# Kernel optimization log

Hardware: AMD Instinct MI355X
Metric: run time of the kernel (lower is better)

Reference implementation:

```python
import jax, jax.numpy as jnp
import numpy as np

N = 50_000
E = 1_600_000
C_IN, C_HID, C_OUT, M = 128, 128, 2, 4


def gcn_norm(edge_index, num_nodes):
    # GCNConv default: add self-loops, symmetric normalization D^-1/2 (A+I) D^-1/2
    src, dst = edge_index[0], edge_index[1]
    loop = jnp.arange(num_nodes, dtype=edge_index.dtype)
    src = jnp.concatenate([src, loop])
    dst = jnp.concatenate([dst, loop])
    deg = jax.ops.segment_sum(jnp.ones_like(dst, dtype=jnp.float32), dst,
                              num_segments=num_nodes)
    dinv = jnp.where(deg > 0, jax.lax.rsqrt(deg), 0.0)
    norm = dinv[src] * dinv[dst]  # [E+N]
    return src, dst, norm


def propagate(h, src, dst, norm, num_nodes):
    # gather -> scale -> scatter-add (the memory-bound core)
    return jax.ops.segment_sum(h[src] * norm[:, None], dst, num_segments=num_nodes)


def setup_inputs() -> dict:
    key = jax.random.key(0)
    k0, k1, k2, k3 = jax.random.split(key, 4)
    x = jax.random.normal(k0, (N, C_IN), dtype=jnp.float32)
    edge_index = jax.random.randint(k1, (2, E), 0, N, dtype=jnp.int32)
    W1 = jax.random.normal(k2, (C_IN, C_HID), dtype=jnp.float32) * (1.0 / np.sqrt(C_IN))
    b1 = jnp.zeros((C_HID,), dtype=jnp.float32)
    W_out = jax.random.normal(k3, (M, C_HID, C_OUT), dtype=jnp.float32) * (1.0 / np.sqrt(C_HID))
    b_out = jnp.zeros((M, C_OUT), dtype=jnp.float32)
    return {"x": x, "edge_index": edge_index, "W1": W1, "b1": b1,
            "W_out": W_out, "b_out": b_out}


def reference(x, edge_index, W1, b1, W_out, b_out):
    n = x.shape[0]
    src, dst, norm = gcn_norm(edge_index, n)
    # hidden GCNConv + ReLU
    h = x @ W1                                  # [N, C_HID]
    h = propagate(h, src, dst, norm, n) + b1    # [N, C_HID]
    h = jax.nn.relu(h)
    # m output GCNConv heads. GCN propagation is linear in features, so
    # A_hat(h W_m) == (A_hat h) W_m: share one graph traversal across heads.
    agg = propagate(h, src, dst, norm, n)       # [N, C_HID]
    out = jnp.einsum('nf,mfo->mno', agg, W_out) + b_out[:, None, :]  # [M, N, C_OUT]
    return out
```

## Files before the change

### kernel.cpp

```cpp
#include <hip/hip_runtime.h>


constexpr int CIN = 128;
constexpr int BSHIFT = 6;
constexpr int NBLKB = 256;
constexpr int NBUK_MAX = 1024;
constexpr int CSR_CAP = 4096;

__device__ inline unsigned pack_bf16x2(float a, float b) {
  unsigned ua = __float_as_uint(a), ub = __float_as_uint(b);
  ua = (ua + 0x7FFFu + ((ua >> 16) & 1u)) >> 16;
  ub = (ub + 0x7FFFu + ((ub >> 16) & 1u)) >> 16;
  return ua | (ub << 16);
}
__device__ inline float bf_lo(unsigned u) { return __uint_as_float(u << 16); }
__device__ inline float bf_hi(unsigned u) { return __uint_as_float(u & 0xFFFF0000u); }

__global__ __launch_bounds__(256) void histbuck_k(const int* __restrict__ dst,
    int* __restrict__ blockhist, int E, int nbuk) {
  __shared__ int lh[NBUK_MAX];
  int b = blockIdx.x, t = threadIdx.x;
  for (int k = t; k < nbuk; k += 256) lh[k] = 0;
  __syncthreads();
  int per = (E + gridDim.x - 1) / gridDim.x;
  int s0 = b * per, s1 = min(E, s0 + per);
  for (int i = s0 + t; i < s1; i += 256) atomicAdd(&lh[dst[i] >> BSHIFT], 1);
  __syncthreads();
  for (int k = t; k < nbuk; k += 256) blockhist[k * NBLKB + b] = lh[k];
}

__global__ void scan_k(const int* __restrict__ v_in,
    int* __restrict__ excl_out, int* __restrict__ btot, int n) {
  __shared__ int wsum[16];
  int t = threadIdx.x, l = t & 63, w = t >> 6;
  int nw = blockDim.x >> 6;
  int i = blockIdx.x * blockDim.x + t;
  int v = (i < n) ? v_in[i] : 0;
  int orig = v;
  #pragma unroll
  for (int off = 1; off < 64; off <<= 1) {
    int u = __shfl_up(v, off);
    if (l >= off) v += u;
  }
  if (l == 63) wsum[w] = v;
  __syncthreads();
  int add = 0;
  for (int j = 0; j < nw; ++j) if (j < w) add += wsum[j];
  v += add;
  if (i < n) excl_out[i] = v - orig;
  if (t == (int)blockDim.x - 1 && btot != nullptr) btot[blockIdx.x] = v;
}

__global__ void scanfix2_k(int* __restrict__ soff, const int* __restrict__ boff, int n) {
  int i = blockIdx.x * 256 + threadIdx.x;
  if (i < n) soff[i] += boff[blockIdx.x];
}

__global__ __launch_bounds__(256) void stageB_k(const int* __restrict__ src,
    const int* __restrict__ dst, const int* __restrict__ soff,
    unsigned* __restrict__ stage, int E, int nbuk) {
  __shared__ int loff[NBUK_MAX];
  int b = blockIdx.x, t = threadIdx.x;
  for (int k = t; k < nbuk; k += 256) loff[k] = soff[k * NBLKB + b];
  __syncthreads();
  int per = (E + gridDim.x - 1) / gridDim.x;
  int s0 = b * per, s1 = min(E, s0 + per);
  for (int i = s0 + t; i < s1; i += 256) {
    int d = dst[i], s = src[i];
    int pos = atomicAdd(&loff[d >> BSHIFT], 1);
    stage[pos] = (unsigned)s | ((unsigned)(d & 63) << 17);
  }
}

__global__ __launch_bounds__(256) void csrloc_k(const unsigned* __restrict__ stage,
    const int* __restrict__ soff, int* __restrict__ row_ptr, int* __restrict__ csr,
    float* __restrict__ dinv, int N, int E, int nbuk) {
  __shared__ int cnt64[64], off64[64], cur64[64];
  __shared__ unsigned ebuf[CSR_CAP];
  __shared__ int sbuf[CSR_CAP];
  int k = blockIdx.x, t = threadIdx.x;
  if (t < 64) { cnt64[t] = 0; cur64[t] = 0; }
  __syncthreads();
  int r0 = soff[k * NBLKB];
  int r1 = (k + 1 < nbuk) ? soff[(k + 1) * NBLKB] : E;
  int len = r1 - r0;
  if (len <= CSR_CAP) {
    for (int i = t; i < len; i += 256) {
      unsigned s = stage[r0 + i];
      ebuf[i] = s;
      atomicAdd(&cnt64[s >> 17], 1);
    }
    __syncthreads();
    if (t < 64) {
      int v = cnt64[t], orig = v;
      #pragma unroll
      for (int off = 1; off < 64; off <<= 1) {
        int u = __shfl_up(v, off);
        if (t >= off) v += u;
      }
      off64[t] = v - orig;
      int n = (k << BSHIFT) + t;
      if (n < N) {
        row_ptr[n] = r0 + v - orig;
        dinv[n] = rsqrtf((float)(orig + 1));
      }
      if (k == nbuk - 1 && t == 63) row_ptr[N] = E;
    }
    __syncthreads();
    for (int i = t; i < len; i += 256) {
      unsigned s = ebuf[i];
      int dl = s >> 17;
      int pos = off64[dl] + atomicAdd(&cur64[dl], 1);
      sbuf[pos] = (int)(s & 0x1FFFF);
    }
    __syncthreads();
    for (int i = t; i < len; i += 256) csr[r0 + i] = sbuf[i];
  } else {
    for (int i = r0 + t; i < r1; i += 256) atomicAdd(&cnt64[stage[i] >> 17], 1);
    __syncthreads();
    if (t < 64) {
      int v = cnt64[t], orig = v;
      #pragma unroll
      for (int off = 1; off < 64; off <<= 1) {
        int u = __shfl_up(v, off);
        if (t >= off) v += u;
      }
      off64[t] = v - orig;
      int n = (k << BSHIFT) + t;
      if (n < N) {
        row_ptr[n] = r0 + v - orig;
        dinv[n] = rsqrtf((float)(orig + 1));
      }
      if (k == nbuk - 1 && t == 63) row_ptr[N] = E;
    }
    __syncthreads();
    for (int i = r0 + t; i < r1; i += 256) {
      unsigned s = stage[i];
      int dl = s >> 17;
      int pos = r0 + off64[dl] + atomicAdd(&cur64[dl], 1);
      csr[pos] = (int)(s & 0x1FFFF);
    }
  }
}

__global__ __launch_bounds__(256) void gemm_k(const float* __restrict__ x,
    const float* __restrict__ W, const float* __restrict__ dinv,
    unsigned* __restrict__ gu, int nrows) {
  __shared__ float As[32][132];
  __shared__ float Bs[32][132];
  int t = threadIdx.x;
  int tx = t & 15, ty = t >> 4;
  int row0 = blockIdx.x * 128;
  float acc[8][8];
  #pragma unroll
  for (int i = 0; i < 8; ++i)
    #pragma unroll
    for (int j = 0; j < 8; ++j) acc[i][j] = 0.f;

  for (int kc = 0; kc < 4; ++kc) {
    int k0 = kc * 32;
    #pragma unroll
    for (int i = 0; i < 4; ++i) {
      int q = t + 256 * i;
      int kq = q & 7, r = q >> 3;
      int grow = row0 + r;
      float4 v = make_float4(0.f, 0.f, 0.f, 0.f);
      if (grow < nrows) v = *(const float4*)&x[grow * CIN + k0 + 4 * kq];
      As[4 * kq + 0][r] = v.x; As[4 * kq + 1][r] = v.y;
      As[4 * kq + 2][r] = v.z; As[4 * kq + 3][r] = v.w;
    }
    #pragma unroll
    for (int i = 0; i < 4; ++i) {
      int q = t + 256 * i;
      int c4 = q & 31, k = q >> 5;
      float4 v = *(const float4*)&W[(k0 + k) * CIN + 4 * c4];
      *(float4*)&Bs[k][4 * c4] = v;
    }
    __syncthreads();
    #pragma unroll
    for (int k = 0; k < 32; ++k) {
      float a[8], b[8];
      *(float4*)&a[0] = *(const float4*)&As[k][4 * ty];
      *(float4*)&a[4] = *(const float4*)&As[k][64 + 4 * ty];
      *(float4*)&b[0] = *(const float4*)&Bs[k][4 * tx];
      *(float4*)&b[4] = *(const float4*)&Bs[k][64 + 4 * tx];
      #pragma unroll
      for (int i = 0; i < 8; ++i)
        #pragma unroll
        for (int j = 0; j < 8; ++j) acc[i][j] = fmaf(a[i], b[j], acc[i][j]);
    }
    __syncthreads();
  }
  #pragma unroll
  for (int i = 0; i < 8; ++i) {
    int r = (i < 4) ? (4 * ty + i) : (64 + 4 * ty + (i - 4));
    int grow = row0 + r;
    if (grow < nrows) {
      float dv = dinv[grow];
      uint2 o0 = make_uint2(pack_bf16x2(acc[i][0] * dv, acc[i][1] * dv),
                            pack_bf16x2(acc[i][2] * dv, acc[i][3] * dv));
      uint2 o1 = make_uint2(pack_bf16x2(acc[i][4] * dv, acc[i][5] * dv),
                            pack_bf16x2(acc[i][6] * dv, acc[i][7] * dv));
      *(uint2*)&gu[grow * 64 + 2 * tx] = o0;
      *(uint2*)&gu[grow * 64 + 32 + 2 * tx] = o1;
    }
  }
}

#define ACC8(U) do { \
  acc[0] += bf_lo((U).x); acc[1] += bf_hi((U).x); \
  acc[2] += bf_lo((U).y); acc[3] += bf_hi((U).y); \
  acc[4] += bf_lo((U).z); acc[5] += bf_hi((U).z); \
  acc[6] += bf_lo((U).w); acc[7] += bf_hi((U).w); } while (0)

__global__ __launch_bounds__(256) void prop1_k(const uint4* __restrict__ g4,
    const int* __restrict__ row_ptr, const int* __restrict__ csr,
    const float* __restrict__ dinv, const float* __restrict__ b1,
    const float* __restrict__ Wout, unsigned* __restrict__ g2w,
    int n_nodes, int n_waves) {
  int l = threadIdx.x & 63;
  int q = l & 15, sub = l >> 4;
  int wid = (blockIdx.x * blockDim.x + threadIdx.x) >> 6;
  float wj0[8], wj1[8], bb[8];
  #pragma unroll
  for (int c = 0; c < 8; ++c) {
    int col = 8 * q + c;
    wj0[c] = Wout[sub * 256 + col * 2];
    wj1[c] = Wout[sub * 256 + col * 2 + 1];
    bb[c] = b1[col];
  }
  for (int n = wid; n < n_nodes; n += n_waves) {
    int start = row_ptr[n], end = row_ptr[n + 1];
    float d = dinv[n];
    float acc[8];
    #pragma unroll
    for (int c = 0; c < 8; ++c) acc[c] = 0.f;
    for (int base = start; base < end; base += 64) {
      int cnt = min(64, end - base);
      int eb = (base + l < end) ? csr[base + l] : 0;
      int i = 0;
      for (; i + 16 <= cnt; i += 16) {
        int s0 = __shfl(eb, i + sub);
        int s1 = __shfl(eb, i + 4 + sub);
        int s2 = __shfl(eb, i + 8 + sub);
        int s3 = __shfl(eb, i + 12 + sub);
        uint4 u0 = g4[s0 * 16 + q];
        uint4 u1 = g4[s1 * 16 + q];
        uint4 u2 = g4[s2 * 16 + q];
        uint4 u3 = g4[s3 * 16 + q];
        ACC8(u0); ACC8(u1); ACC8(u2); ACC8(u3);
      }
      for (; i + 4 <= cnt; i += 4) {
        int s0 = __shfl(eb, i + sub);
        uint4 u0 = g4[s0 * 16 + q];
        ACC8(u0);
      }
      if (i < cnt) {
        int idx = i + sub;
        bool vld = idx < cnt;
        int s0 = __shfl(eb, vld ? idx : i);
        uint4 u0 = g4[s0 * 16 + q];
        if (vld) { ACC8(u0); }
      }
    }
    #pragma unroll
    for (int c = 0; c < 8; ++c) {
      acc[c] += __shfl_xor(acc[c], 16);
      acc[c] += __shfl_xor(acc[c], 32);
    }
    uint4 us = g4[n * 16 + q];
    ACC8(us);
    float p0 = 0.f, p1 = 0.f;
    #pragma unroll
    for (int c = 0; c < 8; ++c) {
      float y = fmaxf(fmaf(acc[c], d, bb[c]), 0.f);
      p0 = fmaf(y, wj0[c], p0);
      p1 = fmaf(y, wj1[c], p1);
    }
    #pragma unroll
    for (int off = 1; off < 16; off <<= 1) {
      p0 += __shfl_xor(p0, off);
      p1 += __shfl_xor(p1, off);
    }
    if (q == 0) g2w[n * 4 + sub] = pack_bf16x2(d * p0, d * p1);
  }
}

__global__ __launch_bounds__(256) void prop2_k(const unsigned short* __restrict__ g2u,
    const int* __restrict__ row_ptr, const int* __restrict__ csr,
    const float* __restrict__ dinv, const float* __restrict__ bout,
    float* __restrict__ out, int n_nodes, int n_groups) {
  int tid = blockIdx.x * blockDim.x + threadIdx.x;
  int gidx = tid >> 3;
  int f = tid & 7;
  float bo = bout[f];
  for (int n = gidx; n < n_nodes; n += n_groups) {
    int start = row_ptr[n], end = row_ptr[n + 1];
    float acc = __uint_as_float(((unsigned)g2u[n * 8 + f]) << 16);
    for (int e = start; e < end; ++e) {
      int s = csr[e];
      acc += __uint_as_float(((unsigned)g2u[s * 8 + f]) << 16);
    }
    out[(f >> 1) * (2 * n_nodes) + n * 2 + (f & 1)] = fmaf(dinv[n], acc, bo);
  }
}

extern "C" void kernel_launch(void* const* d_in, const int* in_sizes, int n_in,
                              void* d_out, int out_size, void* d_ws, size_t ws_size,
                              hipStream_t stream) {
  const float* x    = (const float*)d_in[0];
  const int*   ei   = (const int*)d_in[1];
  const float* W1   = (const float*)d_in[2];
  const float* b1   = (const float*)d_in[3];
  const float* Wout = (const float*)d_in[4];
  const float* bout = (const float*)d_in[5];
  float* out = (float*)d_out;

  const int N = in_sizes[0] / CIN;
  const int E = in_sizes[1] / 2;
  const int* srcp = ei;
  const int* dstp = ei + E;
  const int NBUK = (N + 63) >> BSHIFT;
  const int NSC = NBUK * NBLKB;

  char* ws = (char*)d_ws;
  size_t off = 0;
  auto alloc = [&](size_t bytes) -> void* {
    void* p = ws + off;
    off = (off + bytes + 511) & ~(size_t)511;
    return p;
  };
  unsigned*       gu        = (unsigned*)alloc((size_t)N * 64 * 4);
  unsigned short* g2u       = (unsigned short*)alloc((size_t)N * 8 * 2);
  float*          dinv      = (float*)alloc((size_t)N * 4);
  int*            blockhist = (int*)alloc((size_t)NSC * 4);
  int*            soff      = (int*)alloc((size_t)NSC * 4);
  int*            btot      = (int*)alloc((size_t)NBUK_MAX * 4);
  int*            boff      = (int*)alloc((size_t)NBUK_MAX * 4);
  int*            row_ptr   = (int*)alloc((size_t)(N + 1) * 4);
  int*            csr       = (int*)alloc((size_t)E * 4);
  unsigned*       stage     = (unsigned*)alloc((size_t)E * 4);
  (void)ws_size; (void)n_in; (void)out_size;

  histbuck_k<<<NBLKB, 256, 0, stream>>>(dstp, blockhist, E, NBUK);
  scan_k<<<NBUK, 256, 0, stream>>>(blockhist, soff, btot, NSC);
  scan_k<<<1, 1024, 0, stream>>>(btot, boff, nullptr, NBUK);
  scanfix2_k<<<NBUK, 256, 0, stream>>>(soff, boff, NSC);
  stageB_k<<<NBLKB, 256, 0, stream>>>(srcp, dstp, soff, stage, E, NBUK);
  csrloc_k<<<NBUK, 256, 0, stream>>>(stage, soff, row_ptr, csr, dinv, N, E, NBUK);

  gemm_k<<<(N + 127) / 128, 256, 0, stream>>>(x, W1, dinv, gu, N);

  const int P1_BLOCKS = 2048;
  prop1_k<<<P1_BLOCKS, 256, 0, stream>>>((const uint4*)gu, row_ptr, csr, dinv, b1,
                                         Wout, (unsigned*)g2u, N, P1_BLOCKS * 4);
  const int P2_BLOCKS = 2048;
  prop2_k<<<P2_BLOCKS, 256, 0, stream>>>(g2u, row_ptr, csr, dinv, bout, out,
                                         N, P2_BLOCKS * 32);
}
```

Before: 151.2 us.

## Use split-bf16 MFMA for GEMM, fold scan fixup, vectorize second propagation

Replaces the FP32 FMA GEMM with bf16 MFMA instructions using a hi/lo split (three products) to keep near-FP32 accuracy, with W pre-swizzled in shared memory per block. Removes the scanfix2 kernel by adding the block offset directly in the stageB and csrloc consumers. Rewrites prop2 so each thread handles four output features with 8-byte gathers and a 4-way unrolled edge loop. These changes cut FMA work, one launch, and gather instruction count, at the cost of redundant per-block W conversion and extra MFMA passes for precision.

```diff
diff --git a/kernel.cpp b/kernel.cpp
--- a/kernel.cpp
+++ b/kernel.cpp
@@ -6,6 +6,9 @@
 constexpr int NBLKB = 256;
 constexpr int NBUK_MAX = 1024;
 constexpr int CSR_CAP = 4096;
+
+typedef __attribute__((ext_vector_type(8))) short short8v;
+typedef __attribute__((ext_vector_type(4))) float float4v;
 
 __device__ inline unsigned pack_bf16x2(float a, float b) {
   unsigned ua = __float_as_uint(a), ub = __float_as_uint(b);
@@ -51,17 +54,12 @@
   if (t == (int)blockDim.x - 1 && btot != nullptr) btot[blockIdx.x] = v;
 }
 
-__global__ void scanfix2_k(int* __restrict__ soff, const int* __restrict__ boff, int n) {
-  int i = blockIdx.x * 256 + threadIdx.x;
-  if (i < n) soff[i] += boff[blockIdx.x];
-}
-
 __global__ __launch_bounds__(256) void stageB_k(const int* __restrict__ src,
     const int* __restrict__ dst, const int* __restrict__ soff,
-    unsigned* __restrict__ stage, int E, int nbuk) {
+    const int* __restrict__ boff, unsigned* __restrict__ stage, int E, int nbuk) {
   __shared__ int loff[NBUK_MAX];
   int b = blockIdx.x, t = threadIdx.x;
-  for (int k = t; k < nbuk; k += 256) loff[k] = soff[k * NBLKB + b];
+  for (int k = t; k < nbuk; k += 256) loff[k] = soff[k * NBLKB + b] + boff[k];
   __syncthreads();
   int per = (E + gridDim.x - 1) / gridDim.x;
   int s0 = b * per, s1 = min(E, s0 + per);
@@ -73,7 +71,8 @@
 }
 
 __global__ __launch_bounds__(256) void csrloc_k(const unsigned* __restrict__ stage,
-    const int* __restrict__ soff, int* __restrict__ row_ptr, int* __restrict__ csr,
+    const int* __restrict__ soff, const int* __restrict__ boff,
+    int* __restrict__ row_ptr, int* __restrict__ csr,
     float* __restrict__ dinv, int N, int E, int nbuk) {
   __shared__ int cnt64[64], off64[64], cur64[64];
   __shared__ unsigned ebuf[CSR_CAP];
@@ -81,8 +80,8 @@
   int k = blockIdx.x, t = threadIdx.x;
   if (t < 64) { cnt64[t] = 0; cur64[t] = 0; }
   __syncthreads();
-  int r0 = soff[k * NBLKB];
-  int r1 = (k + 1 < nbuk) ? soff[(k + 1) * NBLKB] : E;
+  int r0 = soff[k * NBLKB] + boff[k];
+  int r1 = (k + 1 < nbuk) ? soff[(k + 1) * NBLKB] + boff[k + 1] : E;
   int len = r1 - r0;
   if (len <= CSR_CAP) {
     for (int i = t; i < len; i += 256) {
@@ -143,66 +142,86 @@
   }
 }
 
+__device__ inline void split8(const float* f, short8v& ah, short8v& al) {
+  #pragma unroll
+  for (int j = 0; j < 8; ++j) {
+    unsigned ua = __float_as_uint(f[j]);
+    unsigned hb = (ua + 0x7FFFu + ((ua >> 16) & 1u)) >> 16;
+    float fh = __uint_as_float(hb << 16);
+    float rl = f[j] - fh;
+    unsigned ub = __float_as_uint(rl);
+    unsigned lb = (ub + 0x7FFFu + ((ub >> 16) & 1u)) >> 16;
+    ah[j] = (short)hb;
+    al[j] = (short)lb;
+  }
+}
+
 __global__ __launch_bounds__(256) void gemm_k(const float* __restrict__ x,
     const float* __restrict__ W, const float* __restrict__ dinv,
     unsigned* __restrict__ gu, int nrows) {
-  __shared__ float As[32][132];
-  __shared__ float Bs[32][132];
-  int t = threadIdx.x;
-  int tx = t & 15, ty = t >> 4;
+  __shared__ unsigned short Bh[16384];
+  __shared__ unsigned short Bl[16384];
+  int t = threadIdx.x, l = t & 63, w = t >> 6;
+  for (int idx = t; idx < 16384; idx += 256) {
+    int k = idx >> 7, col = idx & 127;
+    float wv = W[idx];
+    unsigned ua = __float_as_uint(wv);
+    unsigned hb = (ua + 0x7FFFu + ((ua >> 16) & 1u)) >> 16;
+    float fh = __uint_as_float(hb << 16);
+    float rl = wv - fh;
+    unsigned ub = __float_as_uint(rl);
+    unsigned lb = (ub + 0x7FFFu + ((ub >> 16) & 1u)) >> 16;
+    int addr = (((k >> 5) * 8 + (col >> 4)) * 64 +
+                (((k >> 3) & 3) * 16 + (col & 15))) * 8 + (k & 7);
+    Bh[addr] = (unsigned short)hb;
+    Bl[addr] = (unsigned short)lb;
+  }
+  __syncthreads();
+
   int row0 = blockIdx.x * 128;
-  float acc[8][8];
-  #pragma unroll
-  for (int i = 0; i < 8; ++i)
-    #pragma unroll
-    for (int j = 0; j < 8; ++j) acc[i][j] = 0.f;
-
-  for (int kc = 0; kc < 4; ++kc) {
-    int k0 = kc * 32;
-    #pragma unroll
-    for (int i = 0; i < 4; ++i) {
-      int q = t + 256 * i;
-      int kq = q & 7, r = q >> 3;
-      int grow = row0 + r;
-      float4 v = make_float4(0.f, 0.f, 0.f, 0.f);
-      if (grow < nrows) v = *(const float4*)&x[grow * CIN + k0 + 4 * kq];
-      As[4 * kq + 0][r] = v.x; As[4 * kq + 1][r] = v.y;
-      As[4 * kq + 2][r] = v.z; As[4 * kq + 3][r] = v.w;
-    }
-    #pragma unroll
-    for (int i = 0; i < 4; ++i) {
-      int q = t + 256 * i;
-      int c4 = q & 31, k = q >> 5;
-      float4 v = *(const float4*)&W[(k0 + k) * CIN + 4 * c4];
-      *(float4*)&Bs[k][4 * c4] = v;
-    }
-    __syncthreads();
-    #pragma unroll
-    for (int k = 0; k < 32; ++k) {
-      float a[8], b[8];
-      *(float4*)&a[0] = *(const float4*)&As[k][4 * ty];
-      *(float4*)&a[4] = *(const float4*)&As[k][64 + 4 * ty];
-      *(float4*)&b[0] = *(const float4*)&Bs[k][4 * tx];
-      *(float4*)&b[4] = *(const float4*)&Bs[k][64 + 4 * tx];
+  int ct0 = w * 2;
+  float4v acc[8][2];
+  #pragma unroll
+  for (int i = 0; i < 8; ++i) { acc[i][0] = (float4v)0.f; acc[i][1] = (float4v)0.f; }
+  int arow = row0 + (l & 15);
+  int kln = (l >> 4) * 8;
+
+  for (int ks = 0; ks < 4; ++ks) {
+    short8v bh0 = *(short8v*)&Bh[((ks * 8 + ct0) * 64 + l) * 8];
+    short8v bh1 = *(short8v*)&Bh[((ks * 8 + ct0 + 1) * 64 + l) * 8];
+    short8v bl0 = *(short8v*)&Bl[((ks * 8 + ct0) * 64 + l) * 8];
+    short8v bl1 = *(short8v*)&Bl[((ks * 8 + ct0 + 1) * 64 + l) * 8];
+    #pragma unroll
+    for (int rt = 0; rt < 8; ++rt) {
+      int r = arow + rt * 16;
+      const float* xp = &x[(size_t)min(r, nrows - 1) * CIN + ks * 32 + kln];
+      float f[8];
+      *(float4*)&f[0] = *(const float4*)xp;
+      *(float4*)&f[4] = *(const float4*)(xp + 4);
+      short8v ah, al;
+      split8(f, ah, al);
+      acc[rt][0] = __builtin_amdgcn_mfma_f32_16x16x32_bf16(ah, bh0, acc[rt][0], 0, 0, 0);
+      acc[rt][1] = __builtin_amdgcn_mfma_f32_16x16x32_bf16(ah, bh1, acc[rt][1], 0, 0, 0);
+      acc[rt][0] = __builtin_amdgcn_mfma_f32_16x16x32_bf16(ah, bl0, acc[rt][0], 0, 0, 0);
+      acc[rt][1] = __builtin_amdgcn_mfma_f32_16x16x32_bf16(ah, bl1, acc[rt][1], 0, 0, 0);
+      acc[rt][0] = __builtin_amdgcn_mfma_f32_16x16x32_bf16(al, bh0, acc[rt][0], 0, 0, 0);
+      acc[rt][1] = __builtin_amdgcn_mfma_f32_16x16x32_bf16(al, bh1, acc[rt][1], 0, 0, 0);
+    }
+  }
+  #pragma unroll
+  for (int rt = 0; rt < 8; ++rt) {
+    #pragma unroll
+    for (int r = 0; r < 4; ++r) {
+      int row = row0 + rt * 16 + (l >> 4) * 4 + r;
+      bool ok = row < nrows;
+      float dv = ok ? dinv[row] : 0.f;
       #pragma unroll
-      for (int i = 0; i < 8; ++i)
-        #pragma unroll
-        for (int j = 0; j < 8; ++j) acc[i][j] = fmaf(a[i], b[j], acc[i][j]);
-    }
-    __syncthreads();
-  }
-  #pragma unroll
-  for (int i = 0; i < 8; ++i) {
-    int r = (i < 4) ? (4 * ty + i) : (64 + 4 * ty + (i - 4));
-    int grow = row0 + r;
-    if (grow < nrows) {
-      float dv = dinv[grow];
-      uint2 o0 = make_uint2(pack_bf16x2(acc[i][0] * dv, acc[i][1] * dv),
-                            pack_bf16x2(acc[i][2] * dv, acc[i][3] * dv));
-      uint2 o1 = make_uint2(pack_bf16x2(acc[i][4] * dv, acc[i][5] * dv),
-                            pack_bf16x2(acc[i][6] * dv, acc[i][7] * dv));
-      *(uint2*)&gu[grow * 64 + 2 * tx] = o0;
-      *(uint2*)&gu[grow * 64 + 32 + 2 * tx] = o1;
+      for (int c = 0; c < 2; ++c) {
+        float val = acc[rt][c][r] * dv;
+        float other = __shfl_xor(val, 1);
+        int col = (ct0 + c) * 16 + (l & 15);
+        if (ok && !(l & 1)) gu[(size_t)row * 64 + (col >> 1)] = pack_bf16x2(val, other);
+      }
     }
   }
 }
@@ -286,23 +305,36 @@
   }
 }
 
-__global__ __launch_bounds__(256) void prop2_k(const unsigned short* __restrict__ g2u,
+__global__ __launch_bounds__(256) void prop2_k(const uint2* __restrict__ g2v,
     const int* __restrict__ row_ptr, const int* __restrict__ csr,
     const float* __restrict__ dinv, const float* __restrict__ bout,
-    float* __restrict__ out, int n_nodes, int n_groups) {
-  int tid = blockIdx.x * blockDim.x + threadIdx.x;
-  int gidx = tid >> 3;
-  int f = tid & 7;
-  float bo = bout[f];
-  for (int n = gidx; n < n_nodes; n += n_groups) {
-    int start = row_ptr[n], end = row_ptr[n + 1];
-    float acc = __uint_as_float(((unsigned)g2u[n * 8 + f]) << 16);
-    for (int e = start; e < end; ++e) {
-      int s = csr[e];
-      acc += __uint_as_float(((unsigned)g2u[s * 8 + f]) << 16);
-    }
-    out[(f >> 1) * (2 * n_nodes) + n * 2 + (f & 1)] = fmaf(dinv[n], acc, bo);
-  }
+    float* __restrict__ out, int N) {
+  int tid = blockIdx.x * 256 + threadIdx.x;
+  int n = tid >> 1, hf = tid & 1;
+  if (n >= N) return;
+  uint2 us = g2v[n * 2 + hf];
+  float a0 = bf_lo(us.x), a1 = bf_hi(us.x);
+  float a2 = bf_lo(us.y), a3 = bf_hi(us.y);
+  int e = row_ptr[n], e1 = row_ptr[n + 1];
+  for (; e + 4 <= e1; e += 4) {
+    int i0 = csr[e], i1 = csr[e + 1], i2 = csr[e + 2], i3 = csr[e + 3];
+    uint2 u0 = g2v[i0 * 2 + hf], u1 = g2v[i1 * 2 + hf];
+    uint2 u2 = g2v[i2 * 2 + hf], u3 = g2v[i3 * 2 + hf];
+    a0 += (bf_lo(u0.x) + bf_lo(u1.x)) + (bf_lo(u2.x) + bf_lo(u3.x));
+    a1 += (bf_hi(u0.x) + bf_hi(u1.x)) + (bf_hi(u2.x) + bf_hi(u3.x));
+    a2 += (bf_lo(u0.y) + bf_lo(u1.y)) + (bf_lo(u2.y) + bf_lo(u3.y));
+    a3 += (bf_hi(u0.y) + bf_hi(u1.y)) + (bf_hi(u2.y) + bf_hi(u3.y));
+  }
+  for (; e < e1; ++e) {
+    uint2 u = g2v[csr[e] * 2 + hf];
+    a0 += bf_lo(u.x); a1 += bf_hi(u.x);
+    a2 += bf_lo(u.y); a3 += bf_hi(u.y);
+  }
+  float d = dinv[n];
+  float2 o0 = make_float2(fmaf(d, a0, bout[hf * 4 + 0]), fmaf(d, a1, bout[hf * 4 + 1]));
+  float2 o1 = make_float2(fmaf(d, a2, bout[hf * 4 + 2]), fmaf(d, a3, bout[hf * 4 + 3]));
+  *(float2*)&out[(size_t)(hf * 2 + 0) * (2 * N) + 2 * n] = o0;
+  *(float2*)&out[(size_t)(hf * 2 + 1) * (2 * N) + 2 * n] = o1;
 }
 
 extern "C" void kernel_launch(void* const* d_in, const int* in_sizes, int n_in,
@@ -345,16 +377,14 @@
   histbuck_k<<<NBLKB, 256, 0, stream>>>(dstp, blockhist, E, NBUK);
   scan_k<<<NBUK, 256, 0, stream>>>(blockhist, soff, btot, NSC);
   scan_k<<<1, 1024, 0, stream>>>(btot, boff, nullptr, NBUK);
-  scanfix2_k<<<NBUK, 256, 0, stream>>>(soff, boff, NSC);
-  stageB_k<<<NBLKB, 256, 0, stream>>>(srcp, dstp, soff, stage, E, NBUK);
-  csrloc_k<<<NBUK, 256, 0, stream>>>(stage, soff, row_ptr, csr, dinv, N, E, NBUK);
+  stageB_k<<<NBLKB, 256, 0, stream>>>(srcp, dstp, soff, boff, stage, E, NBUK);
+  csrloc_k<<<NBUK, 256, 0, stream>>>(stage, soff, boff, row_ptr, csr, dinv, N, E, NBUK);
 
   gemm_k<<<(N + 127) / 128, 256, 0, stream>>>(x, W1, dinv, gu, N);
 
   const int P1_BLOCKS = 2048;
   prop1_k<<<P1_BLOCKS, 256, 0, stream>>>((const uint4*)gu, row_ptr, csr, dinv, b1,
                                          Wout, (unsigned*)g2u, N, P1_BLOCKS * 4);
-  const int P2_BLOCKS = 2048;
-  prop2_k<<<P2_BLOCKS, 256, 0, stream>>>(g2u, row_ptr, csr, dinv, bout, out,
-                                         N, P2_BLOCKS * 32);
-}
+  prop2_k<<<(2 * N + 255) / 256, 256, 0, stream>>>((const uint2*)g2u, row_ptr, csr,
+                                                   dinv, bout, out, N);
+}
```

Measured after the change: 144.1 us. 4.7% less time.
